# Kernel tuning notes

Measured on AMD Instinct MI355X. Metric: run time of the kernel, lower is better.

Reference implementation:

```python
import jax, jax.numpy as jnp
import numpy as np

T = 1024      # tokens
H = 2048      # hidden_size
I = 1408      # moe_intermediate_size
E = 16        # n_routed_experts
K = 6         # num_experts_per_tok
SI = I * 2    # shared experts intermediate (n_shared_experts=2)


def setup_inputs() -> dict:
    key = jax.random.key(0)
    ks = jax.random.split(key, 8)
    s = 0.02
    return {
        "x": jax.random.normal(ks[0], (T, H), jnp.float32),
        "gate_w": jax.random.normal(ks[1], (E, H), jnp.float32) * s,
        "w_gate": jax.random.normal(ks[2], (E, I, H), jnp.float32) * s,
        "w_up": jax.random.normal(ks[3], (E, I, H), jnp.float32) * s,
        "w_down": jax.random.normal(ks[4], (E, H, I), jnp.float32) * s,
        "sw_gate": jax.random.normal(ks[5], (SI, H), jnp.float32) * s,
        "sw_up": jax.random.normal(ks[6], (SI, H), jnp.float32) * s,
        "sw_down": jax.random.normal(ks[7], (H, SI), jnp.float32) * s,
    }


def reference(x, gate_w, w_gate, w_up, w_down, sw_gate, sw_up, sw_down):
    t = x.shape[0]
    # ---- router: softmax over experts, top-k, renormalize (norm_topk_prob) ----
    logits = x @ gate_w.T                                   # [T, E]
    probs = jax.nn.softmax(logits.astype(jnp.float32), axis=-1)
    topw, topi = jax.lax.top_k(probs, K)                    # [T, K]
    topw = topw / jnp.sum(topw, axis=-1, keepdims=True)
    # per-token per-expert combine weight (0 for unselected experts)
    comb = jnp.zeros((t, E), probs.dtype).at[
        jnp.arange(t)[:, None], topi
    ].add(topw)                                             # [T, E]

    # ---- routed experts: SwiGLU MLP per expert, weighted combine ----
    g = jnp.einsum('th,eih->tei', x, w_gate)                # [T, E, I]
    u = jnp.einsum('th,eih->tei', x, w_up)                  # [T, E, I]
    h = jax.nn.silu(g) * u                                  # [T, E, I]
    routed = jnp.einsum('te,tei,ehi->th', comb, h, w_down)  # [T, H]

    # ---- shared experts (always-on SwiGLU MLP) ----
    shared = (jax.nn.silu(x @ sw_gate.T) * (x @ sw_up.T)) @ sw_down.T  # [T, H]

    return routed + shared
```

## Files before the change

kernel.cpp:

```cpp
#include <hip/hip_runtime.h>
#include <stdint.h>

#define T_TOK 1024
#define H_DIM 2048
#define I_DIM 1408
#define E_NUM 16
#define K_TOP 6
#define PADCAP 8192
#define NE_ALL 18

typedef __attribute__((ext_vector_type(8))) short short8;
typedef __attribute__((ext_vector_type(8))) unsigned short ushort8;
typedef __attribute__((ext_vector_type(4))) float f32x4;

__device__ __forceinline__ unsigned short f2b(float f) {
    unsigned u = __float_as_uint(f);
    u += 0x7fffu + ((u >> 16) & 1u);
    return (unsigned short)(u >> 16);
}
__device__ __forceinline__ float b2f(unsigned short s) {
    return __uint_as_float((unsigned)s << 16);
}

__device__ __forceinline__ unsigned cvt_pk2(float a, float b) {
    unsigned r;
    asm("v_cvt_pk_bf16_f32 %0, %1, %2" : "=v"(r) : "v"(a), "v"(b));
    return r;
}

typedef __attribute__((address_space(1))) const unsigned int as1_uint;
typedef __attribute__((address_space(3))) unsigned int as3_uint;
__device__ __forceinline__ void gload16(const void* g, void* l) {
    __builtin_amdgcn_global_load_lds((as1_uint*)g, (as3_uint*)l, 16, 0, 0);
}

#define SCHED0() __builtin_amdgcn_sched_barrier(0)
#define RBAR() __builtin_amdgcn_s_barrier()

__device__ __forceinline__ int xcd_swizzle(int bid, int nwg) {
    const int q = nwg >> 3, r = nwg & 7;
    const int xcd = bid & 7, k = bid >> 3;
    const int base = (xcd < r) ? xcd * (q + 1) : r * (q + 1) + (xcd - r) * q;
    return base + k;
}

__global__ __launch_bounds__(256) void router_kernel(
    const float* __restrict__ x, const float* __restrict__ gw,
    float* __restrict__ topw, int* __restrict__ eidx, int* __restrict__ slotarr,
    int* __restrict__ counts)
{
    const int t = blockIdx.x, tid = threadIdx.x;
    const int lane = tid & 63, wave = tid >> 6;
    float part[E_NUM];
#pragma unroll
    for (int e = 0; e < E_NUM; ++e) part[e] = 0.f;
    const float* xr = x + (size_t)t * H_DIM;
    for (int i = tid; i < H_DIM; i += 256) {
        float xv = xr[i];
#pragma unroll
        for (int e = 0; e < E_NUM; ++e) part[e] += xv * gw[e * H_DIM + i];
    }
    __shared__ float red[4][E_NUM];
#pragma unroll
    for (int e = 0; e < E_NUM; ++e) {
        float v = part[e];
        for (int off = 32; off; off >>= 1) v += __shfl_down(v, off);
        if (lane == 0) red[wave][e] = v;
    }
    __syncthreads();
    if (tid == 0) {
        float logits[E_NUM];
#pragma unroll
        for (int e = 0; e < E_NUM; ++e)
            logits[e] = red[0][e] + red[1][e] + red[2][e] + red[3][e];
        int sel[K_TOP]; float selv[K_TOP];
        unsigned used = 0;
        for (int k = 0; k < K_TOP; ++k) {
            int best = 0; float bv = -1e30f;
            for (int e = 0; e < E_NUM; ++e)
                if (!((used >> e) & 1u) && logits[e] > bv) { bv = logits[e]; best = e; }
            used |= 1u << best; sel[k] = best; selv[k] = bv;
        }
        float mx = selv[0], s = 0.f, w[K_TOP];
        for (int k = 0; k < K_TOP; ++k) { w[k] = expf(selv[k] - mx); s += w[k]; }
        float inv = 1.f / s;
        for (int k = 0; k < K_TOP; ++k) {
            int slot = atomicAdd(&counts[sel[k]], 1);
            topw[t * K_TOP + k] = w[k] * inv;
            eidx[t * K_TOP + k] = sel[k];
            slotarr[t * K_TOP + k] = slot;
        }
    }
}

__global__ void zero_counts_kernel(int* counts) {
    if (threadIdx.x < E_NUM) counts[threadIdx.x] = 0;
}

__global__ void prefix_kernel(const int* __restrict__ counts, int* __restrict__ offs) {
    if (threadIdx.x == 0) {
        int o = 0;
        for (int e = 0; e < E_NUM; ++e) { offs[e] = o; o += (counts[e] + 127) & ~127; }
        offs[E_NUM] = o;
    }
}

__global__ __launch_bounds__(256) void gather_cvt_kernel(
    const float* __restrict__ x, const int* __restrict__ eidx,
    const int* __restrict__ slotarr, const int* __restrict__ offs,
    ushort* __restrict__ Xall)
{
    const int b = blockIdx.x;
    int t; size_t row;
    if (b < T_TOK * K_TOP) {
        t = b / K_TOP;
        row = (size_t)offs[eidx[b]] + (size_t)slotarr[b];
    } else {
        t = b - T_TOK * K_TOP;
        row = (size_t)offs[E_NUM] + (size_t)t;
    }
    const float* src = x + (size_t)t * H_DIM;
    ushort* dst = Xall + row * H_DIM;
    const int i = threadIdx.x * 8;
    float4 f0 = *(const float4*)(src + i);
    float4 f1 = *(const float4*)(src + i + 4);
    ushort8 v;
    v[0] = f2b(f0.x); v[1] = f2b(f0.y); v[2] = f2b(f0.z); v[3] = f2b(f0.w);
    v[4] = f2b(f1.x); v[5] = f2b(f1.y); v[6] = f2b(f1.z); v[7] = f2b(f1.w);
    *(ushort8*)(dst + i) = v;
}

template<int DOWN>
__global__ __launch_bounds__(256, 3) void moe_gemm_kernel(
    const ushort* __restrict__ Abase,
    const float* __restrict__ Wr1, const float* __restrict__ Wr2,
    const float* __restrict__ Ws1, const float* __restrict__ Ws2,
    ushort* __restrict__ C1, ushort* __restrict__ C2,
    const int* __restrict__ counts, const int* __restrict__ offs,
    int nNT, int lda, int K, int ldc)
{
    __shared__ short Alds[2][128 * 64];
    __shared__ short Blds[128 * 64];

    const int work = xcd_swizzle(blockIdx.x, gridDim.x);
    const int slab = NE_ALL * 8;
    int nt = work / slab;
    const int rem = work - nt * slab;
    const int e = rem >> 3;
    const int mt = rem & 7;

    const int S = offs[E_NUM];
    const int M = (e < E_NUM) ? counts[e] : 1024;
    const int row0 = mt << 7;
    if (row0 >= M) return;
    const int crowbase = (e < E_NUM) ? offs[e] : S + ((e - E_NUM) << 10);
    const int arowbase = DOWN ? crowbase : ((e < E_NUM) ? offs[e] : S);

    const float* B; ushort* C; int ldb, koff = 0;
    if (DOWN) {
        C = C1;
        if (e < E_NUM) { ldb = I_DIM; B = Wr1 + (size_t)e * H_DIM * I_DIM; }
        else           { ldb = 2 * I_DIM; B = Ws1; koff = (e - E_NUM) * I_DIM; }
    } else {
        ldb = H_DIM;
        const float* Bg = (e < E_NUM) ? Wr1 + (size_t)e * I_DIM * H_DIM
                                      : Ws1 + (size_t)(e - E_NUM) * I_DIM * H_DIM;
        const float* Bu = (e < E_NUM) ? Wr2 + (size_t)e * I_DIM * H_DIM
                                      : Ws2 + (size_t)(e - E_NUM) * I_DIM * H_DIM;
        if (nt < nNT) { B = Bg; C = C1; } else { B = Bu; C = C2; nt -= nNT; }
    }
    const int n0 = nt << 7;

    const int tid = threadIdx.x;
    const int lane = tid & 63;
    const int wave = tid >> 6;
    const int wm = wave & 1, wn = wave >> 1;
    const int l15 = lane & 15, lhi = lane >> 4;

    const char* __restrict__ Ab = (const char*)(Abase + (size_t)(arowbase + row0) * lda);

    int aOff[4];
#pragma unroll
    for (int i = 0; i < 4; ++i) {
        const int chunk = wave * 4 + i;
        const int off = chunk * 1024 + lane * 16;
        const int r = off >> 7, s = (off >> 4) & 7;
        aOff[i] = r * lda * 2 + ((s ^ (r & 7)) << 4);
    }

    const int br_ = tid >> 3, bs = tid & 7;
    const float* Bc[4]; int bldw[4];
#pragma unroll
    for (int i = 0; i < 4; ++i) {
        const int r = br_ + (i << 5);
        Bc[i] = B + (size_t)(n0 + r) * ldb + koff + (bs << 3);
        bldw[i] = (r << 6) + ((bs ^ (r & 7)) << 3);
    }

    f32x4 acc[4][4];
#pragma unroll
    for (int m = 0; m < 4; ++m)
#pragma unroll
        for (int n = 0; n < 4; ++n) acc[m][n] = (f32x4){0.f, 0.f, 0.f, 0.f};

    float4 br[4][2];

    auto issueB = [&](int kt) {
#pragma unroll
        for (int i = 0; i < 4; ++i) {
            const float* src = Bc[i] + (kt << 6);
            br[i][0] = *(const float4*)src;
            br[i][1] = *(const float4*)(src + 4);
        }
    };
    auto issueA = [&](int kt, int pb) {
#pragma unroll
        for (int i = 0; i < 4; ++i)
            gload16(Ab + (size_t)aOff[i] + (size_t)(kt << 7),
                    (char*)Alds[pb] + (wave * 4 + i) * 1024);
    };
    auto writeB = [&]() {
#pragma unroll
        for (int i = 0; i < 4; ++i) {
            union { short8 s; unsigned u[4]; } w;
            w.u[0] = cvt_pk2(br[i][0].x, br[i][0].y);
            w.u[1] = cvt_pk2(br[i][0].z, br[i][0].w);
            w.u[2] = cvt_pk2(br[i][1].x, br[i][1].y);
            w.u[3] = cvt_pk2(br[i][1].z, br[i][1].w);
            *(short8*)&Blds[bldw[i]] = w.s;
        }
    };
    auto compute = [&](int p) {
#pragma unroll
        for (int kk = 0; kk < 2; ++kk) {
            const int kb = (kk << 2) + lhi;
            short8 af[4], bfr[4];
#pragma unroll
            for (int m = 0; m < 4; ++m) {
                const int rA = (wm << 6) + (m << 4) + l15;
                af[m] = *(const short8*)&Alds[p][(rA << 6) + ((kb ^ (rA & 7)) << 3)];
            }
#pragma unroll
            for (int n = 0; n < 4; ++n) {
                const int rB = (wn << 6) + (n << 4) + l15;
                bfr[n] = *(const short8*)&Blds[(rB << 6) + ((kb ^ (rB & 7)) << 3)];
            }
            __builtin_amdgcn_s_setprio(1);
#pragma unroll
            for (int m = 0; m < 4; ++m)
#pragma unroll
                for (int n = 0; n < 4; ++n)
                    acc[m][n] = __builtin_amdgcn_mfma_f32_16x16x32_bf16(
                        af[m], bfr[n], acc[m][n], 0, 0, 0);
            __builtin_amdgcn_s_setprio(0);
        }
    };

    const int nK = K >> 6;
    issueB(0); SCHED0();
    issueA(0, 0); SCHED0();
    writeB();
    asm volatile("s_waitcnt vmcnt(0) lgkmcnt(0)" ::: "memory");
    RBAR(); SCHED0();

    int p = 0;
    for (int kt = 0; kt < nK; ++kt) {
        const bool more = (kt + 1 < nK);
        if (more) {
            issueB(kt + 1); SCHED0();
            issueA(kt + 1, p ^ 1); SCHED0();
        }
        compute(p);
        if (more) {
            RBAR();
            writeB();
            asm volatile("s_waitcnt vmcnt(0) lgkmcnt(0)" ::: "memory");
            RBAR(); SCHED0();
            p ^= 1;
        }
    }

    const size_t cbase_col = (size_t)n0 + (wn << 6) + l15;
#pragma unroll
    for (int m = 0; m < 4; ++m) {
        const int rloc = (wm << 6) + (m << 4) + (lhi << 2);
#pragma unroll
        for (int j = 0; j < 4; ++j) {
            const int crow = row0 + rloc + j;
            if (crow >= M) continue;
            const size_t co = (size_t)(crowbase + crow) * ldc + cbase_col;
#pragma unroll
            for (int n = 0; n < 4; ++n) C[co + (n << 4)] = f2b(acc[m][n][j]);
        }
    }
}

__global__ __launch_bounds__(256) void silu_kernel(
    ushort* __restrict__ G, const ushort* __restrict__ U,
    const int* __restrict__ eidx, const int* __restrict__ slotarr,
    const int* __restrict__ offs)
{
    const int b = blockIdx.x;
    size_t row;
    if (b < T_TOK * K_TOP) {
        row = (size_t)offs[eidx[b]] + (size_t)slotarr[b];
    } else {
        row = (size_t)offs[E_NUM] + (size_t)(b - T_TOK * K_TOP);
    }
    ushort* g = G + row * I_DIM;
    const ushort* u = U + row * I_DIM;
    const int i = threadIdx.x * 8;
    if (i < I_DIM) {
        ushort8 gv = *(const ushort8*)(g + i);
        ushort8 uv = *(const ushort8*)(u + i);
        ushort8 hv;
#pragma unroll
        for (int j = 0; j < 8; ++j) {
            float gf = b2f(gv[j]);
            float uf = b2f(uv[j]);
            float sf = gf / (1.f + expf(-gf));
            hv[j] = f2b(sf * uf);
        }
        *(ushort8*)(g + i) = hv;
    }
}

__global__ __launch_bounds__(256) void combine_kernel(
    float* __restrict__ out, const ushort* __restrict__ Y,
    const float* __restrict__ topw, const int* __restrict__ eidx,
    const int* __restrict__ slotarr, const int* __restrict__ offs)
{
    const int t = blockIdx.x;
    const int i = threadIdx.x * 8;
    const int S = offs[E_NUM];
    float acc[8];
    {
        ushort8 v0 = *(const ushort8*)(Y + ((size_t)S + t) * H_DIM + i);
        ushort8 v1 = *(const ushort8*)(Y + ((size_t)S + 1024 + t) * H_DIM + i);
#pragma unroll
        for (int j = 0; j < 8; ++j) acc[j] = b2f(v0[j]) + b2f(v1[j]);
    }
#pragma unroll
    for (int k = 0; k < K_TOP; ++k) {
        const float w = topw[t * K_TOP + k];
        const size_t row = (size_t)offs[eidx[t * K_TOP + k]] + (size_t)slotarr[t * K_TOP + k];
        ushort8 v = *(const ushort8*)(Y + row * H_DIM + i);
#pragma unroll
        for (int j = 0; j < 8; ++j) acc[j] += w * b2f(v[j]);
    }
    float* o = out + (size_t)t * H_DIM;
    float4 o0, o1;
    o0.x = acc[0]; o0.y = acc[1]; o0.z = acc[2]; o0.w = acc[3];
    o1.x = acc[4]; o1.y = acc[5]; o1.z = acc[6]; o1.w = acc[7];
    *(float4*)(o + i) = o0;
    *(float4*)(o + i + 4) = o1;
}

extern "C" void kernel_launch(void* const* d_in, const int* in_sizes, int n_in,
                              void* d_out, int out_size, void* d_ws, size_t ws_size,
                              hipStream_t stream) {
    const float* x       = (const float*)d_in[0];
    const float* gate_w  = (const float*)d_in[1];
    const float* w_gate  = (const float*)d_in[2];
    const float* w_up    = (const float*)d_in[3];
    const float* w_down  = (const float*)d_in[4];
    const float* sw_gate = (const float*)d_in[5];
    const float* sw_up   = (const float*)d_in[6];
    const float* sw_down = (const float*)d_in[7];
    float* out = (float*)d_out;

    char* p = (char*)d_ws;
    auto take = [&](size_t b) { char* r = p; p += (b + 255) & ~(size_t)255; return r; };
    int*    counts = (int*)take(32 * 4);
    int*    offs   = (int*)take(32 * 4);
    float*  topw   = (float*)take((size_t)T_TOK * K_TOP * 4);
    int*    eidx   = (int*)take((size_t)T_TOK * K_TOP * 4);
    int*    slot   = (int*)take((size_t)T_TOK * K_TOP * 4);
    ushort* Xall   = (ushort*)take((size_t)(PADCAP + 1024) * H_DIM * 2);
    ushort* G      = (ushort*)take((size_t)(PADCAP + 2048) * I_DIM * 2);
    ushort* U      = (ushort*)take((size_t)(PADCAP + 2048) * I_DIM * 2);
    ushort* Y      = (ushort*)take((size_t)(PADCAP + 2048) * H_DIM * 2);

    zero_counts_kernel<<<1, 64, 0, stream>>>(counts);
    router_kernel<<<T_TOK, 256, 0, stream>>>(x, gate_w, topw, eidx, slot, counts);
    prefix_kernel<<<1, 64, 0, stream>>>(counts, offs);
    gather_cvt_kernel<<<T_TOK * K_TOP + T_TOK, 256, 0, stream>>>(x, eidx, slot, offs, Xall);

    moe_gemm_kernel<0><<<22 * NE_ALL * 8, 256, 0, stream>>>(
        Xall, w_gate, w_up, sw_gate, sw_up, G, U, counts, offs,
        11, H_DIM , H_DIM , I_DIM );
    silu_kernel<<<T_TOK * K_TOP + 2048, 256, 0, stream>>>(G, U, eidx, slot, offs);
    moe_gemm_kernel<1><<<16 * NE_ALL * 8, 256, 0, stream>>>(
        G, w_down, nullptr, sw_down, nullptr, Y, nullptr, counts, offs,
        16, I_DIM , I_DIM , H_DIM );

    combine_kernel<<<T_TOK, 256, 0, stream>>>(out, Y, topw, eidx, slot, offs);
}
```

Baseline: 468.1 us.

## Prefetch B two tiles ahead with partial waits and expert-major tile order

The GEMM main loop now double-buffers the fp32 weight registers, so the global loads for tile k+2 are issued while tile k is computed. The wait before each barrier uses vmcnt(8) instead of draining all loads, which leaves the next B prefetch in flight. Work indices are also remapped to an expert-major order so blocks of the same expert sit next to each other, which may change how well weight and activation tiles are reused in cache. The cost is more register pressure under the 3-waves launch bound, and the loop assumes an even tile count, relying on clamped indices and an exact vmcnt ordering.

```diff
diff --git a/kernel.cpp b/kernel.cpp
--- a/kernel.cpp
+++ b/kernel.cpp
@@ -36,6 +36,7 @@
 
 #define SCHED0() __builtin_amdgcn_sched_barrier(0)
 #define RBAR() __builtin_amdgcn_s_barrier()
+#define WAIT_A() asm volatile("s_waitcnt vmcnt(8) lgkmcnt(0)" ::: "memory")
 
 __device__ __forceinline__ int xcd_swizzle(int bid, int nwg) {
     const int q = nwg >> 3, r = nwg & 7;
@@ -137,16 +138,16 @@
     const float* __restrict__ Ws1, const float* __restrict__ Ws2,
     ushort* __restrict__ C1, ushort* __restrict__ C2,
     const int* __restrict__ counts, const int* __restrict__ offs,
-    int nNT, int lda, int K, int ldc)
+    int nNT, int totNT, int lda, int K, int ldc)
 {
     __shared__ short Alds[2][128 * 64];
     __shared__ short Blds[128 * 64];
 
     const int work = xcd_swizzle(blockIdx.x, gridDim.x);
-    const int slab = NE_ALL * 8;
-    int nt = work / slab;
-    const int rem = work - nt * slab;
-    const int e = rem >> 3;
+    const int perE = totNT * 8;
+    const int e = work / perE;
+    const int rem = work - e * perE;
+    int nt = rem >> 3;
     const int mt = rem & 7;
 
     const int S = offs[E_NUM];
@@ -203,9 +204,15 @@
 #pragma unroll
         for (int n = 0; n < 4; ++n) acc[m][n] = (f32x4){0.f, 0.f, 0.f, 0.f};
 
-    float4 br[4][2];
-
-    auto issueB = [&](int kt) {
+    float4 brA[4][2], brB[4][2];
+
+    auto issueA = [&](int kt, int pb) {
+#pragma unroll
+        for (int i = 0; i < 4; ++i)
+            gload16(Ab + (size_t)aOff[i] + (size_t)(kt << 7),
+                    (char*)Alds[pb] + (wave * 4 + i) * 1024);
+    };
+    auto issueB = [&](int kt, float4 (&br)[4][2]) {
 #pragma unroll
         for (int i = 0; i < 4; ++i) {
             const float* src = Bc[i] + (kt << 6);
@@ -213,13 +220,7 @@
             br[i][1] = *(const float4*)(src + 4);
         }
     };
-    auto issueA = [&](int kt, int pb) {
-#pragma unroll
-        for (int i = 0; i < 4; ++i)
-            gload16(Ab + (size_t)aOff[i] + (size_t)(kt << 7),
-                    (char*)Alds[pb] + (wave * 4 + i) * 1024);
-    };
-    auto writeB = [&]() {
+    auto writeB = [&](float4 (&br)[4][2]) {
 #pragma unroll
         for (int i = 0; i < 4; ++i) {
             union { short8 s; unsigned u[4]; } w;
@@ -257,27 +258,29 @@
     };
 
     const int nK = K >> 6;
-    issueB(0); SCHED0();
     issueA(0, 0); SCHED0();
-    writeB();
+    issueB(0, brB); SCHED0();
+    writeB(brB);
+    issueB(nK > 1 ? 1 : 0, brA);
     asm volatile("s_waitcnt vmcnt(0) lgkmcnt(0)" ::: "memory");
     RBAR(); SCHED0();
 
-    int p = 0;
-    for (int kt = 0; kt < nK; ++kt) {
-        const bool more = (kt + 1 < nK);
-        if (more) {
-            issueB(kt + 1); SCHED0();
-            issueA(kt + 1, p ^ 1); SCHED0();
-        }
-        compute(p);
-        if (more) {
-            RBAR();
-            writeB();
-            asm volatile("s_waitcnt vmcnt(0) lgkmcnt(0)" ::: "memory");
-            RBAR(); SCHED0();
-            p ^= 1;
-        }
+    for (int tt = 0; tt < nK; tt += 2) {
+        issueA(min(tt + 1, nK - 1), 1); SCHED0();
+        issueB(min(tt + 2, nK - 1), brB); SCHED0();
+        compute(0);
+        RBAR();
+        writeB(brA);
+        WAIT_A(); SCHED0();
+        RBAR(); SCHED0();
+
+        issueA(min(tt + 2, nK - 1), 0); SCHED0();
+        issueB(min(tt + 3, nK - 1), brA); SCHED0();
+        compute(1);
+        RBAR();
+        writeB(brB);
+        WAIT_A(); SCHED0();
+        RBAR(); SCHED0();
     }
 
     const size_t cbase_col = (size_t)n0 + (wn << 6) + l15;
@@ -386,13 +389,13 @@
     prefix_kernel<<<1, 64, 0, stream>>>(counts, offs);
     gather_cvt_kernel<<<T_TOK * K_TOP + T_TOK, 256, 0, stream>>>(x, eidx, slot, offs, Xall);
 
-    moe_gemm_kernel<0><<<22 * NE_ALL * 8, 256, 0, stream>>>(
+    moe_gemm_kernel<0><<<NE_ALL * 22 * 8, 256, 0, stream>>>(
         Xall, w_gate, w_up, sw_gate, sw_up, G, U, counts, offs,
-        11, H_DIM , H_DIM , I_DIM );
+        11, 22, H_DIM , H_DIM , I_DIM );
     silu_kernel<<<T_TOK * K_TOP + 2048, 256, 0, stream>>>(G, U, eidx, slot, offs);
-    moe_gemm_kernel<1><<<16 * NE_ALL * 8, 256, 0, stream>>>(
+    moe_gemm_kernel<1><<<NE_ALL * 16 * 8, 256, 0, stream>>>(
         G, w_down, nullptr, sw_down, nullptr, Y, nullptr, counts, offs,
-        16, I_DIM , I_DIM , H_DIM );
+        16, 16, I_DIM , I_DIM , H_DIM );
 
     combine_kernel<<<T_TOK, 256, 0, stream>>>(out, Y, topw, eidx, slot, offs);
 }
```

After: 1.775 ms. 3.79x slower.
